# Optimization experiments

Measured on AMD Instinct MI355X. Metric: run time of the kernel, lower is better.

Reference implementation:

```python
import jax, jax.numpy as jnp
import numpy as np

N_EMBD = 768
N_HEAD = 12
HEAD_DIM = N_EMBD // N_HEAD


def setup_inputs() -> dict:
    key = jax.random.key(0)
    ks = jax.random.split(key, 9)
    s = 0.02
    return {
        "x": jax.random.normal(ks[0], (2, 4096, N_EMBD), dtype=jnp.float32),
        "Wq": jax.random.normal(ks[1], (N_EMBD, N_EMBD), dtype=jnp.float32) * s,
        "bq": jnp.zeros((N_EMBD,), dtype=jnp.float32),
        "Wk": jax.random.normal(ks[2], (N_EMBD, N_EMBD), dtype=jnp.float32) * s,
        "bk": jnp.zeros((N_EMBD,), dtype=jnp.float32),
        "Wv": jax.random.normal(ks[3], (N_EMBD, N_EMBD), dtype=jnp.float32) * s,
        "bv": jnp.zeros((N_EMBD,), dtype=jnp.float32),
        "Wo": jax.random.normal(ks[4], (N_EMBD, N_EMBD), dtype=jnp.float32) * s,
        "bo": jnp.zeros((N_EMBD,), dtype=jnp.float32),
    }


def reference(x, Wq, bq, Wk, bk, Wv, bv, Wo, bo):
    B, T, C = x.shape
    H, D = N_HEAD, HEAD_DIM
    # torch Linear: y = x @ W.T + b
    q = (x @ Wq.T + bq).reshape(B, T, H, D).transpose(0, 2, 1, 3)  # [B,H,T,D]
    k = (x @ Wk.T + bk).reshape(B, T, H, D).transpose(0, 2, 1, 3)
    v = (x @ Wv.T + bv).reshape(B, T, H, D).transpose(0, 2, 1, 3)
    scale = 1.0 / jnp.sqrt(jnp.float32(D))
    att = jnp.einsum("bhqd,bhkd->bhqk", q, k) * scale  # [B,H,T,T]
    causal = jnp.tril(jnp.ones((T, T), dtype=bool))
    att = jnp.where(causal[None, None], att, -jnp.inf)
    att = jax.nn.softmax(att, axis=-1)
    y = jnp.einsum("bhqk,bhkd->bhqd", att, v)
    y = y.transpose(0, 2, 1, 3).reshape(B, T, C)
    return y @ Wo.T + bo
```

## Files before the change

kernel.cpp:

```cpp
#include <hip/hip_runtime.h>

typedef __bf16 bf16_t;
typedef __bf16 bf16x4 __attribute__((ext_vector_type(4)));
typedef __bf16 bf16x8 __attribute__((ext_vector_type(8)));
typedef float  f32x4  __attribute__((ext_vector_type(4)));
typedef float  f32x16 __attribute__((ext_vector_type(16)));
typedef unsigned int u32;

#define MFMA16(a, b, c) __builtin_amdgcn_mfma_f32_16x16x32_bf16((a), (b), (c), 0, 0, 0)
#define MFMA32(a, b, c) __builtin_amdgcn_mfma_f32_32x32x16_bf16((a), (b), (c), 0, 0, 0)

__device__ __forceinline__ void gld_lds16(const bf16_t* g, bf16_t* l) {
  __builtin_amdgcn_global_load_lds((__attribute__((address_space(1))) void*)g,
                                   (__attribute__((address_space(3))) void*)l, 16, 0, 0);
}
__device__ __forceinline__ u32 cvt_pk_bf16(float lo, float hi) {
  u32 r;
  asm("v_cvt_pk_bf16_f32 %0, %1, %2" : "=v"(r) : "v"(lo), "v"(hi));
  return r;
}

__global__ void cast_f32_bf16(const float* __restrict__ s, bf16_t* __restrict__ d, int n) {
  int i = (blockIdx.x * blockDim.x + threadIdx.x) * 4;
  if (i >= n) return;
  float4 v = *(const float4*)(s + i);
  bf16x4 o;
  o[0] = (bf16_t)v.x; o[1] = (bf16_t)v.y; o[2] = (bf16_t)v.z; o[3] = (bf16_t)v.w;
  *(bf16x4*)(d + i) = o;
}

__global__ void prep_w(const float* __restrict__ Wq, const float* __restrict__ Wk,
                       const float* __restrict__ Wv, const float* __restrict__ Wo,
                       const float* __restrict__ bq, const float* __restrict__ bk,
                       const float* __restrict__ bv,
                       bf16_t* __restrict__ wqkv, bf16_t* __restrict__ wob,
                       float* __restrict__ qkvb) {
  const int NW = 768 * 768;
  const int t = blockIdx.x * 256 + threadIdx.x;
  const int i = t * 4;
  if (i < 3 * NW) {
    const float* s; int off;
    if (i < NW)          { s = Wq; off = i; }
    else if (i < 2 * NW) { s = Wk; off = i - NW; }
    else                 { s = Wv; off = i - 2 * NW; }
    float4 v = *(const float4*)(s + off);
    bf16x4 o;
    o[0] = (bf16_t)v.x; o[1] = (bf16_t)v.y; o[2] = (bf16_t)v.z; o[3] = (bf16_t)v.w;
    *(bf16x4*)(wqkv + i) = o;
  } else if (i < 4 * NW) {
    const int off = i - 3 * NW;
    float4 v = *(const float4*)(Wo + off);
    bf16x4 o;
    o[0] = (bf16_t)v.x; o[1] = (bf16_t)v.y; o[2] = (bf16_t)v.z; o[3] = (bf16_t)v.w;
    *(bf16x4*)(wob + off) = o;
  }
  if (t < 2304) qkvb[t] = t < 768 ? bq[t] : (t < 1536 ? bk[t - 768] : bv[t - 1536]);
}

__global__ __launch_bounds__(256) void gemm_qkv(
    const bf16_t* __restrict__ A, const bf16_t* __restrict__ B,
    const float* __restrict__ bias,
    bf16_t* __restrict__ qb, bf16_t* __restrict__ kb2, bf16_t* __restrict__ vtb) {
  __shared__ __align__(16) bf16_t As[128 * 64];
  __shared__ __align__(16) bf16_t Bs[128 * 64];
  const int K = 768;
  const int p = blockIdx.x;
  const int xcd = p & 7, u = p >> 3;
  const int bm = xcd * 8 + u / 18;
  const int bn = u - (u / 18) * 18;
  const int tid = threadIdx.x;
  const int w = tid >> 6, l = tid & 63, lg = l >> 4, ln = l & 15;
  const int wr = w >> 1, wc = w & 1;
  const int lr8 = l >> 3, lc8 = l & 7;
  const int region = (bn * 128) / 768;
  const int ln7 = ln & 7;
  f32x4 acc[4][4] = {};
  if (region != 2) {
    for (int kb = 0; kb < K / 64; ++kb) {
      const int k0 = kb * 64;
#pragma unroll
      for (int i = 0; i < 4; ++i) {
        const int row = w * 32 + i * 8 + lr8;
        const int so = k0 + ((lc8 ^ (row & 7)) << 3);
        gld_lds16(A + (size_t)(bm * 128 + row) * K + so, As + (w * 32 + i * 8) * 64 + l * 8);
        gld_lds16(B + (size_t)(bn * 128 + row) * K + so, Bs + (w * 32 + i * 8) * 64 + l * 8);
      }
      __syncthreads();
#pragma unroll
      for (int kk = 0; kk < 2; ++kk) {
        bf16x8 af[4], bfr[4];
#pragma unroll
        for (int m = 0; m < 4; ++m) {
          const int jc = ((kk * 4 + lg) ^ ln7) << 3;
          af[m]  = *(const bf16x8*)(As + (wr * 64 + m * 16 + ln) * 64 + jc);
          bfr[m] = *(const bf16x8*)(Bs + (wc * 64 + m * 16 + ln) * 64 + jc);
        }
#pragma unroll
        for (int m = 0; m < 4; ++m)
#pragma unroll
          for (int n = 0; n < 4; ++n) acc[m][n] = MFMA16(af[m], bfr[n], acc[m][n]);
      }
      __syncthreads();
    }
    const float scl = (region == 0) ? 0.18033688011112042f : 1.0f;
    bf16_t* dst = region == 0 ? qb : kb2;
#pragma unroll
    for (int m = 0; m < 4; ++m)
#pragma unroll
      for (int n = 0; n < 4; ++n)
#pragma unroll
        for (int j = 0; j < 4; ++j) {
          const int gm = bm * 128 + wr * 64 + m * 16 + lg * 4 + j;
          const int gn = bn * 128 + wc * 64 + n * 16 + ln;
          const float v = (acc[m][n][j] + bias[gn]) * scl;
          const int c = gn - region * 768;
          const int bb = gm >> 12, tt = gm & 4095;
          const int hh = c >> 6, d = c & 63;
          dst[((size_t)(bb * 12 + hh) * 4096 + tt) * 64 + d] = (bf16_t)v;
        }
  } else {
    for (int kb = 0; kb < K / 64; ++kb) {
      const int k0 = kb * 64;
#pragma unroll
      for (int i = 0; i < 4; ++i) {
        const int row = w * 32 + i * 8 + lr8;
        const int so = k0 + ((lc8 ^ (row & 7)) << 3);
        gld_lds16(A + (size_t)(bm * 128 + row) * K + so, As + (w * 32 + i * 8) * 64 + l * 8);
        gld_lds16(B + (size_t)(bn * 128 + row) * K + so, Bs + (w * 32 + i * 8) * 64 + l * 8);
      }
      __syncthreads();
#pragma unroll
      for (int kk = 0; kk < 2; ++kk) {
        bf16x8 af[4], bfr[4];
#pragma unroll
        for (int m = 0; m < 4; ++m) {
          const int jc = ((kk * 4 + lg) ^ ln7) << 3;
          af[m]  = *(const bf16x8*)(As + (wr * 64 + m * 16 + ln) * 64 + jc);
          bfr[m] = *(const bf16x8*)(Bs + (wc * 64 + m * 16 + ln) * 64 + jc);
        }
#pragma unroll
        for (int m = 0; m < 4; ++m)
#pragma unroll
          for (int n = 0; n < 4; ++n) acc[m][n] = MFMA16(bfr[n], af[m], acc[m][n]);
      }
      __syncthreads();
    }
#pragma unroll
    for (int m = 0; m < 4; ++m)
#pragma unroll
      for (int n = 0; n < 4; ++n)
#pragma unroll
        for (int j = 0; j < 4; ++j) {
          const int gn = bn * 128 + wc * 64 + n * 16 + lg * 4 + j;
          const int gm = bm * 128 + wr * 64 + m * 16 + ln;
          const float v = acc[m][n][j] + bias[gn];
          const int c = gn - 1536;
          const int bb = gm >> 12, tt = gm & 4095;
          const int hh = c >> 6, d = c & 63;
          vtb[((size_t)(bb * 12 + hh) * 64 + d) * 4096 + tt] = (bf16_t)v;
        }
  }
}

__global__ __launch_bounds__(512) void attn_fwd(
    const bf16_t* __restrict__ q, const bf16_t* __restrict__ k,
    const bf16_t* __restrict__ vt, bf16_t* __restrict__ y) {
  __shared__ __align__(16) unsigned char SMEM[33280];
  bf16_t* Ks = (bf16_t*)SMEM;
  bf16_t* Vs = (bf16_t*)(SMEM + 16384);
  float*  osh = (float*)SMEM;
  float*  lsh = (float*)(SMEM + 32768);

  const int p = blockIdx.x;
  const int xcd = p & 7, slot = p >> 3;
  const int hb = xcd + 8 * (slot % 3);
  const int qt = 31 - slot / 3;
  const int tid = threadIdx.x;
  const int w = tid >> 6, l = tid & 63, lq = l & 31, lh = l >> 5;
  const int wq = w >> 1, wc = w & 1;
  const size_t hbo = (size_t)hb * (4096 * 64);
  const bf16_t* qh = q + hbo;
  const bf16_t* kh = k + hbo;
  const bf16_t* vh = vt + hbo;

  const int q0 = qt * 128 + wq * 32;
  const int qidx = q0 + lq;
  const int nst = 2 * qt + 2;

  const int sr = ((tid >> 8) << 5) | (tid & 31);
  const int sc = ((((tid >> 6) & 3) << 1) | ((tid >> 5) & 1)) << 3;
  const bf16_t* ksrc = kh + ((size_t)sr * 64 + sc);
  const bf16_t* vsrc = vh + ((size_t)sr * 4096 + sc);

  bf16x8 qf[4];
#pragma unroll
  for (int ds = 0; ds < 4; ++ds)
    qf[ds] = *(const bf16x8*)(qh + (size_t)qidx * 64 + 16 * ds + 8 * lh);
  bf16x8 ones;
#pragma unroll
  for (int j = 0; j < 8; ++j) ones[j] = (bf16_t)1.0f;

  gld_lds16(ksrc, Ks + tid * 8);
  gld_lds16(vsrc, Vs + tid * 8);
  __syncthreads();

  f32x16 o0 = {}, o1 = {}, osum = {};

  int cur = 0;
  for (int t = 0; t < nst; ++t) {
    if (t + 1 < nst) {
      gld_lds16(ksrc + 4096, Ks + (cur ^ 1) * 4096 + tid * 8);
      gld_lds16(vsrc + 64, Vs + (cur ^ 1) * 4096 + tid * 8);
    }
    ksrc += 4096; vsrc += 64;
    const int kvb = t * 64;
    if (kvb <= q0 + 31) {
      const bool diag = (kvb + 63 > q0);
      const bf16_t* KsW = Ks + cur * 4096;
      const bf16_t* VsW = Vs + cur * 4096;
      f32x16 st = {};
      __builtin_amdgcn_s_setprio(1);
#pragma unroll
      for (int ds = 0; ds < 4; ++ds) {
        bf16x8 kf = *(const bf16x8*)(KsW + (wc * 4 + ds) * 512 + l * 8);
        st = MFMA32(kf, qf[ds], st);
      }
      __builtin_amdgcn_s_setprio(0);
      float pv[16];
#pragma unroll
      for (int r = 0; r < 16; ++r) pv[r] = __builtin_amdgcn_exp2f(st[r]);
      if (diag) {
        const int kb0 = kvb + wc * 32 + 4 * lh;
#pragma unroll
        for (int r = 0; r < 16; ++r)
          if (kb0 + (r & 3) + 8 * (r >> 2) > qidx) pv[r] = 0.f;
      }
      u32 pq[8];
#pragma unroll
      for (int g = 0; g < 8; ++g) pq[g] = cvt_pk_bf16(pv[2 * g], pv[2 * g + 1]);
#pragma unroll
      for (int ks2 = 0; ks2 < 2; ++ks2) {
        asm("v_permlane32_swap_b32 %0, %1" : "+v"(pq[4 * ks2 + 0]), "+v"(pq[4 * ks2 + 2]));
        asm("v_permlane32_swap_b32 %0, %1" : "+v"(pq[4 * ks2 + 1]), "+v"(pq[4 * ks2 + 3]));
      }
      __builtin_amdgcn_s_setprio(1);
#pragma unroll
      for (int ks = 0; ks < 2; ++ks) {
        bf16x8 pa = *(const bf16x8*)&pq[ks * 4];
        bf16x8 v0 = *(const bf16x8*)(VsW + (2 * wc + ks) * 512 + l * 8);
        bf16x8 v1 = *(const bf16x8*)(VsW + (4 + 2 * wc + ks) * 512 + l * 8);
        o0 = MFMA32(pa, v0, o0);
        o1 = MFMA32(pa, v1, o1);
        osum = MFMA32(pa, ones, osum);
      }
      __builtin_amdgcn_s_setprio(0);
    }
    __syncthreads();
    cur ^= 1;
  }

  if (wc == 1) {
#pragma unroll
    for (int r = 0; r < 16; ++r) {
      osh[wq * 2048 + r * 64 + l] = o0[r];
      osh[wq * 2048 + (16 + r) * 64 + l] = o1[r];
    }
    if (lq == 0) {
#pragma unroll
      for (int r = 0; r < 16; ++r)
        lsh[wq * 32 + (r & 3) + 8 * (r >> 2) + 4 * lh] = osum[r];
    }
  }
  __syncthreads();
  if (wc == 0) {
#pragma unroll
    for (int r = 0; r < 16; ++r) {
      o0[r] += osh[wq * 2048 + r * 64 + l];
      o1[r] += osh[wq * 2048 + (16 + r) * 64 + l];
    }
    float linv[16];
#pragma unroll
    for (int r = 0; r < 16; ++r) {
      const int rl = (r & 3) + 8 * (r >> 2) + 4 * lh;
      linv[r] = 1.0f / (osum[r] + lsh[wq * 32 + rl]);
    }
    const int b = hb / 12, h = hb - b * 12;
#pragma unroll
    for (int r = 0; r < 16; ++r) {
      const int row = q0 + (r & 3) + 8 * (r >> 2) + 4 * lh;
      bf16_t* yr = y + ((size_t)b * 4096 + row) * 768 + h * 64 + lq;
      yr[0]  = (bf16_t)(o0[r] * linv[r]);
      yr[32] = (bf16_t)(o1[r] * linv[r]);
    }
  }
}

__global__ __launch_bounds__(256) void gemm_out(
    const bf16_t* __restrict__ A, const bf16_t* __restrict__ B,
    const float* __restrict__ bias, float* __restrict__ out) {
  __shared__ __align__(16) bf16_t As[64 * 64];
  __shared__ __align__(16) bf16_t Bs[128 * 64];
  const int K = 768;
  const int p = blockIdx.x;
  const int xcd = p & 7, u = p >> 3;
  const int bm = xcd * 16 + u / 6;
  const int bn = u - (u / 6) * 6;
  const int tid = threadIdx.x;
  const int w = tid >> 6, l = tid & 63, lg = l >> 4, ln = l & 15;
  const int lr8 = l >> 3, lc8 = l & 7;
  const int ln7 = ln & 7;
  f32x4 acc[4][2] = {};
  for (int kb = 0; kb < K / 64; ++kb) {
    const int k0 = kb * 64;
#pragma unroll
    for (int i = 0; i < 2; ++i) {
      const int row = w * 16 + i * 8 + lr8;
      const int so = k0 + ((lc8 ^ (row & 7)) << 3);
      gld_lds16(A + (size_t)(bm * 64 + row) * K + so, As + (w * 16 + i * 8) * 64 + l * 8);
    }
#pragma unroll
    for (int i = 0; i < 4; ++i) {
      const int row = w * 32 + i * 8 + lr8;
      const int so = k0 + ((lc8 ^ (row & 7)) << 3);
      gld_lds16(B + (size_t)(bn * 128 + row) * K + so, Bs + (w * 32 + i * 8) * 64 + l * 8);
    }
    __syncthreads();
#pragma unroll
    for (int kk = 0; kk < 2; ++kk) {
      const int jc = ((kk * 4 + lg) ^ ln7) << 3;
      bf16x8 af[4], bfr[2];
#pragma unroll
      for (int m = 0; m < 4; ++m)
        af[m] = *(const bf16x8*)(As + (m * 16 + ln) * 64 + jc);
#pragma unroll
      for (int n = 0; n < 2; ++n)
        bfr[n] = *(const bf16x8*)(Bs + (w * 32 + n * 16 + ln) * 64 + jc);
#pragma unroll
      for (int m = 0; m < 4; ++m)
#pragma unroll
        for (int n = 0; n < 2; ++n) acc[m][n] = MFMA16(af[m], bfr[n], acc[m][n]);
    }
    __syncthreads();
  }
#pragma unroll
  for (int m = 0; m < 4; ++m) {
#pragma unroll
    for (int n = 0; n < 2; ++n) {
#pragma unroll
      for (int j = 0; j < 4; ++j) {
        const int gm = bm * 64 + m * 16 + lg * 4 + j;
        const int gn = bn * 128 + w * 32 + n * 16 + ln;
        out[(size_t)gm * 768 + gn] = acc[m][n][j] + bias[gn];
      }
    }
  }
}

extern "C" void kernel_launch(void* const* d_in, const int* in_sizes, int n_in,
                              void* d_out, int out_size, void* d_ws, size_t ws_size,
                              hipStream_t stream) {
  const float* x  = (const float*)d_in[0];
  const float* Wq = (const float*)d_in[1];
  const float* bq = (const float*)d_in[2];
  const float* Wk = (const float*)d_in[3];
  const float* bk = (const float*)d_in[4];
  const float* Wv = (const float*)d_in[5];
  const float* bv = (const float*)d_in[6];
  const float* Wo = (const float*)d_in[7];
  const float* bo = (const float*)d_in[8];
  float* out = (float*)d_out;

  const int M = 8192, C = 768, QKV = 2304;
  bf16_t* xb   = (bf16_t*)d_ws;
  bf16_t* wqkv = xb + (size_t)M * C;
  bf16_t* wob  = wqkv + (size_t)QKV * C;
  float*  qkvb = (float*)(wob + (size_t)C * C);
  bf16_t* qbuf = (bf16_t*)(qkvb + QKV);
  bf16_t* kbuf = qbuf + (size_t)M * C;
  bf16_t* vtb  = kbuf + (size_t)M * C;
  bf16_t* yb   = xb;

  cast_f32_bf16<<<6144, 256, 0, stream>>>(x, xb, M * C);
  prep_w<<<2304, 256, 0, stream>>>(Wq, Wk, Wv, Wo, bq, bk, bv, wqkv, wob, qkvb);

  gemm_qkv<<<1152, 256, 0, stream>>>(xb, wqkv, qkvb, qbuf, kbuf, vtb);
  attn_fwd<<<768, 512, 0, stream>>>(qbuf, kbuf, vtb, yb);
  gemm_out<<<768, 256, 0, stream>>>(yb, wob, bo, out);
}
```

Baseline: 150.5 us.

## Halve attention block query tile to 64 rows with 256-thread blocks

The attention kernel now processes 64 query rows per block with 4 waves instead of 128 rows with 8 waves, and launches twice as many blocks. Each thread now issues two K and two V global-to-LDS loads per stage to fill the same 64-key tile. The aim is finer-grained causal work distribution, less wasted work on diagonal tiles, and possibly higher occupancy. The cost is that K/V tiles are reloaded from memory twice as often overall, and the per-block reduction/epilogue code that was written for 8 waves must still be correct with 4.

```diff
diff --git a/kernel.cpp b/kernel.cpp
--- a/kernel.cpp
+++ b/kernel.cpp
@@ -162,7 +162,7 @@
   }
 }
 
-__global__ __launch_bounds__(512) void attn_fwd(
+__global__ __launch_bounds__(256) void attn_fwd(
     const bf16_t* __restrict__ q, const bf16_t* __restrict__ k,
     const bf16_t* __restrict__ vt, bf16_t* __restrict__ y) {
   __shared__ __align__(16) unsigned char SMEM[33280];
@@ -174,7 +174,7 @@
   const int p = blockIdx.x;
   const int xcd = p & 7, slot = p >> 3;
   const int hb = xcd + 8 * (slot % 3);
-  const int qt = 31 - slot / 3;
+  const int q64 = 63 - slot / 3;
   const int tid = threadIdx.x;
   const int w = tid >> 6, l = tid & 63, lq = l & 31, lh = l >> 5;
   const int wq = w >> 1, wc = w & 1;
@@ -183,14 +183,16 @@
   const bf16_t* kh = k + hbo;
   const bf16_t* vh = vt + hbo;
 
-  const int q0 = qt * 128 + wq * 32;
+  const int q0 = q64 * 64 + wq * 32;
   const int qidx = q0 + lq;
-  const int nst = 2 * qt + 2;
-
-  const int sr = ((tid >> 8) << 5) | (tid & 31);
-  const int sc = ((((tid >> 6) & 3) << 1) | ((tid >> 5) & 1)) << 3;
-  const bf16_t* ksrc = kh + ((size_t)sr * 64 + sc);
-  const bf16_t* vsrc = vh + ((size_t)sr * 4096 + sc);
+  const int nst = q64 + 1;
+
+  const int sr0 = tid & 31;
+  const int sc0 = ((((tid >> 6) & 3) << 1) | ((tid >> 5) & 1)) << 3;
+  const bf16_t* kA = kh + ((size_t)sr0 * 64 + sc0);
+  const bf16_t* kB = kh + ((size_t)(sr0 + 32) * 64 + sc0);
+  const bf16_t* vA = vh + ((size_t)sr0 * 4096 + sc0);
+  const bf16_t* vB = vh + ((size_t)(sr0 + 32) * 4096 + sc0);
 
   bf16x8 qf[4];
 #pragma unroll
@@ -200,8 +202,10 @@
 #pragma unroll
   for (int j = 0; j < 8; ++j) ones[j] = (bf16_t)1.0f;
 
-  gld_lds16(ksrc, Ks + tid * 8);
-  gld_lds16(vsrc, Vs + tid * 8);
+  gld_lds16(kA, Ks + tid * 8);
+  gld_lds16(kB, Ks + 2048 + tid * 8);
+  gld_lds16(vA, Vs + tid * 8);
+  gld_lds16(vB, Vs + 2048 + tid * 8);
   __syncthreads();
 
   f32x16 o0 = {}, o1 = {}, osum = {};
@@ -209,10 +213,14 @@
   int cur = 0;
   for (int t = 0; t < nst; ++t) {
     if (t + 1 < nst) {
-      gld_lds16(ksrc + 4096, Ks + (cur ^ 1) * 4096 + tid * 8);
-      gld_lds16(vsrc + 64, Vs + (cur ^ 1) * 4096 + tid * 8);
-    }
-    ksrc += 4096; vsrc += 64;
+      bf16_t* kd = Ks + (cur ^ 1) * 4096;
+      bf16_t* vd = Vs + (cur ^ 1) * 4096;
+      gld_lds16(kA + 4096, kd + tid * 8);
+      gld_lds16(kB + 4096, kd + 2048 + tid * 8);
+      gld_lds16(vA + 64, vd + tid * 8);
+      gld_lds16(vB + 64, vd + 2048 + tid * 8);
+    }
+    kA += 4096; kB += 4096; vA += 64; vB += 64;
     const int kvb = t * 64;
     if (kvb <= q0 + 31) {
       const bool diag = (kvb + 63 > q0);
@@ -384,6 +392,6 @@
   prep_w<<<2304, 256, 0, stream>>>(Wq, Wk, Wv, Wo, bq, bk, bv, wqkv, wob, qkvb);
 
   gemm_qkv<<<1152, 256, 0, stream>>>(xb, wqkv, qkvb, qbuf, kbuf, vtb);
-  attn_fwd<<<768, 512, 0, stream>>>(qbuf, kbuf, vtb, yb);
+  attn_fwd<<<1536, 256, 0, stream>>>(qbuf, kbuf, vtb, yb);
   gemm_out<<<768, 256, 0, stream>>>(yb, wob, bo, out);
 }
```

Measured after the change: 184.4 us. 22.5% more time.
